# Kernel optimization log

Measured on AMD Instinct MI355X. Metric: run time of the kernel, lower is better.

## Reference

```python
import jax, jax.numpy as jnp
import numpy as np

N_ENT = 100000
N_REL = 500
IN_DIM = 128
OUT_DIM = 128
E = 500000


def setup_inputs() -> dict:
    key = jax.random.key(0)
    ks = jax.random.split(key, 9)
    src = jax.random.randint(ks[0], (E,), 0, N_ENT)
    dst = jax.random.randint(ks[1], (E,), 0, N_ENT)
    rel = jax.random.randint(ks[2], (E,), 0, N_REL)
    ent_embed = jax.random.normal(ks[3], (N_ENT, IN_DIM), dtype=jnp.float32)
    rel_embed = jax.random.normal(ks[4], (N_REL, IN_DIM), dtype=jnp.float32)
    # xavier_normal with gain 1.414 for linear weights
    g = 1.414
    a_w = jax.random.normal(ks[5], (OUT_DIM, 3 * IN_DIM), dtype=jnp.float32) * (g * np.sqrt(2.0 / (3 * IN_DIM + OUT_DIM)))
    a_b = jnp.zeros((OUT_DIM,), dtype=jnp.float32)
    a2_w = jax.random.normal(ks[6], (1, OUT_DIM), dtype=jnp.float32) * (g * np.sqrt(2.0 / (OUT_DIM + 1)))
    a2_b = jnp.zeros((1,), dtype=jnp.float32)
    return {"ent_embed": ent_embed, "rel_embed": rel_embed, "a_w": a_w, "a_b": a_b,
            "a2_w": a2_w, "a2_b": a2_b, "src": src, "dst": dst, "rel": rel}


def reference(ent_embed, rel_embed, a_w, a_b, a2_w, a2_b, src, dst, rel):
    # gather: [E, 3*in_dim]
    h = jnp.concatenate([ent_embed[src], ent_embed[dst], rel_embed[rel]], axis=1)
    c = h @ a_w.T + a_b                      # [E, out_dim]
    b = jax.nn.leaky_relu(c @ a2_w.T + a2_b, negative_slope=0.01)  # [E, 1]
    e_b = jnp.exp(b)                          # [E, 1]
    temp1 = e_b * c                           # [E, out_dim]
    # scatter-sum into source nodes (SpecialSpmmFinal keyed on edges[0] = src)
    e_b_sum = jax.ops.segment_sum(e_b, src, num_segments=N_ENT)   # [N, 1]
    h_sum = jax.ops.segment_sum(temp1, src, num_segments=N_ENT)   # [N, out_dim]
    ebs = jnp.where(e_b_sum == 0, jnp.float32(1e-12), e_b_sum)
    h_ent = h_sum / ebs
    # scatter-mean of temp1 by relation id
    rel_sum = jax.ops.segment_sum(temp1, rel, num_segments=N_REL)          # [R, out_dim]
    rel_cnt = jax.ops.segment_sum(jnp.ones((temp1.shape[0],), jnp.float32), rel, num_segments=N_REL)
    h_rel = rel_sum / jnp.maximum(rel_cnt, 1.0)[:, None]
    return (jax.nn.elu(h_ent), jax.nn.elu(h_rel))
```

## Files before the change

kernel.cpp:

```cpp
#include <hip/hip_runtime.h>
#include <hip/hip_bf16.h>

#define N_ENT_C 100000
#define N_REL_C 500
#define NEDGE_C 500000
#define SCAN_BLOCKS 391
#define EPB 1024
#define NB_EDGE 489
#define CHUNK_B 62
#define MT_TOTAL 6250
#define MT_PER_BLOCK 8
#define MFMA_GRID 782
#define CVT_GRID 1563

#define OFF_WTHI  0
#define OFF_WTLO  16384
#define OFF_WTR   32768
#define OFF_PR    49152
#define OFF_PRH   113152
#define OFF_QR    145920
#define OFF_QS    146432
#define OFF_QD    246432
#define OFF_OSRC  346432
#define OFF_DSTS  446432
#define OFF_RELS  946432
#define OFF_PSH   1446432
#define OFF_PDH   7846432

#define DO_HSRC     0
#define DO_BSUM     100000
#define DO_RELSTART 100512
#define DO_PART8    101024
#define DO_CHUNKOFF 105120
#define DO_BLKHIST  109216
#define DO_BLKOFFS  359584
#define DO_SRCR     609952
#define DO_DSTR     1109952
#define DO_RELP     1609952

typedef short bf16x8 __attribute__((ext_vector_type(8)));
typedef float f32x4  __attribute__((ext_vector_type(4)));
typedef unsigned short u16x8 __attribute__((ext_vector_type(8)));

__device__ inline unsigned short bf_rne(float x) {
    unsigned int u = __float_as_uint(x);
    u += 0x7FFF + ((u >> 16) & 1);
    return (unsigned short)(u >> 16);
}
__device__ inline float bf2f(unsigned short h) {
    return __uint_as_float(((unsigned int)h) << 16);
}

__global__ void prep_w(const float* __restrict__ aw, unsigned short* __restrict__ Wthi,
                       unsigned short* __restrict__ Wtlo, float* __restrict__ Wtr) {
    int idx = blockIdx.x * 256 + threadIdx.x;
    if (idx < 32768) {
        int n = idx >> 7, k = idx & 127;
        float v = (n < 128) ? aw[n * 384 + k] : aw[(n - 128) * 384 + 128 + k];
        unsigned short h = bf_rne(v);
        Wthi[idx] = h;
        Wtlo[idx] = bf_rne(v - bf2f(h));
    } else if (idx < 49152) {
        int t = idx - 32768;
        int k = t >> 7, o = t & 127;
        Wtr[t] = aw[o * 384 + 256 + k];
    }
}

__global__ void rel_proj(const float* __restrict__ rele, const float* __restrict__ Wtr,
                         const float* __restrict__ ab, const float* __restrict__ a2w,
                         float* __restrict__ Pr, unsigned short* __restrict__ PrH,
                         float* __restrict__ qr) {
    int r = blockIdx.x;
    int o = threadIdx.x;
    float acc = ab[o];
    for (int k = 0; k < 128; ++k)
        acc = fmaf(rele[r * 128 + k], Wtr[k * 128 + o], acc);
    Pr[r * 128 + o] = acc;
    PrH[r * 128 + o] = bf_rne(acc);
    __shared__ float red[128];
    red[o] = acc * a2w[o];
    __syncthreads();
    for (int off = 64; off > 0; off >>= 1) {
        if (o < off) red[o] += red[o + off];
        __syncthreads();
    }
    if (o == 0) qr[r] = red[0];
}

__global__ __launch_bounds__(256) void ent_cvt(const float* __restrict__ ent,
                                               uint4* __restrict__ EntF) {
    int gw = blockIdx.x * 256 + threadIdx.x;
    int mt = gw >> 6;
    if (mt >= MT_TOTAL) return;
    int lane = gw & 63;
    int row = mt * 16 + (lane & 15);
    int kb0 = (lane >> 4) * 8;
    const float* rp = ent + (size_t)row * 128;
    size_t mb = (size_t)mt * 8;
#pragma unroll
    for (int ks = 0; ks < 4; ++ks) {
        float4 a = *(const float4*)(rp + ks * 32 + kb0);
        float4 b = *(const float4*)(rp + ks * 32 + kb0 + 4);
        float f[8] = {a.x, a.y, a.z, a.w, b.x, b.y, b.z, b.w};
        union { unsigned short u[8]; uint4 v; } H, L;
#pragma unroll
        for (int j = 0; j < 8; ++j) {
            unsigned short h = bf_rne(f[j]);
            H.u[j] = h;
            L.u[j] = bf_rne(f[j] - bf2f(h));
        }
        EntF[(mb + ks) * 64 + lane] = H.v;
        EntF[(mb + 4 + ks) * 64 + lane] = L.v;
    }
}

__global__ __launch_bounds__(512, 4) void ent_mfma3(const uint4* __restrict__ EntF,
                                                    const unsigned short* __restrict__ Wthi,
                                                    const unsigned short* __restrict__ Wtlo,
                                                    const float* __restrict__ a2w,
                                                    unsigned short* __restrict__ PsH,
                                                    unsigned short* __restrict__ PdH,
                                                    float* __restrict__ qs,
                                                    float* __restrict__ qd) {
    const int tid = threadIdx.x;
    const int w = tid >> 6, lane = tid & 63;
    const int l15 = lane & 15, lh = lane >> 4;
    const int n0 = w * 32;

    bf16x8 wh[2][4], wl[2][4];
#pragma unroll
    for (int nf = 0; nf < 2; ++nf) {
        int n = n0 + nf * 16 + l15;
#pragma unroll
        for (int ks = 0; ks < 4; ++ks) {
            int kb = ks * 32 + lh * 8;
            wh[nf][ks] = *(const bf16x8*)(Wthi + n * 128 + kb);
            wl[nf][ks] = *(const bf16x8*)(Wtlo + n * 128 + kb);
        }
    }
#pragma unroll
    for (int nf = 0; nf < 2; ++nf)
#pragma unroll
        for (int ks = 0; ks < 4; ++ks) {
            asm volatile("" : "+v"(wh[nf][ks]));
            asm volatile("" : "+v"(wl[nf][ks]));
        }

    float a2v[2][4];
#pragma unroll
    for (int nf = 0; nf < 2; ++nf)
#pragma unroll
        for (int v = 0; v < 4; ++v)
            a2v[nf][v] = a2w[(n0 + nf * 16 + lh * 4 + v) & 127];

    const bool isPs = (w < 4);
    unsigned short* PH = isPs ? PsH : PdH;
    float* qout = isPs ? qs : qd;
    const int colbase = (n0 & 127) + lh * 4;

    const bf16x8* EB = (const bf16x8*)EntF;
    f32x4 zz = {0.f, 0.f, 0.f, 0.f};
    const int mt0 = blockIdx.x * MT_PER_BLOCK;

#pragma unroll
    for (int i = 0; i < MT_PER_BLOCK; ++i) {
        int mt = mt0 + i;
        if (mt >= MT_TOTAL) break;
        size_t mb = (size_t)mt * 512;
        bf16x8 eh[4], el[4];
#pragma unroll
        for (int ks = 0; ks < 4; ++ks) {
            eh[ks] = EB[mb + (size_t)ks * 64 + lane];
            el[ks] = EB[mb + 256 + (size_t)ks * 64 + lane];
        }
        f32x4 acc[2];
        acc[0] = zz; acc[1] = zz;
#pragma unroll
        for (int ks = 0; ks < 4; ++ks)
#pragma unroll
            for (int nf = 0; nf < 2; ++nf) {
                acc[nf] = __builtin_amdgcn_mfma_f32_16x16x32_bf16(wh[nf][ks], eh[ks], acc[nf], 0, 0, 0);
                acc[nf] = __builtin_amdgcn_mfma_f32_16x16x32_bf16(wh[nf][ks], el[ks], acc[nf], 0, 0, 0);
                acc[nf] = __builtin_amdgcn_mfma_f32_16x16x32_bf16(wl[nf][ks], eh[ks], acc[nf], 0, 0, 0);
            }

        int m = mt * 16 + l15;
        float qp = 0.f;
#pragma unroll
        for (int nf = 0; nf < 2; ++nf) {
            ushort4 st;
            st.x = bf_rne(acc[nf][0]);
            st.y = bf_rne(acc[nf][1]);
            st.z = bf_rne(acc[nf][2]);
            st.w = bf_rne(acc[nf][3]);
#pragma unroll
            for (int v = 0; v < 4; ++v) qp = fmaf(acc[nf][v], a2v[nf][v], qp);
            *(ushort4*)&PH[(size_t)m * 128 + colbase + nf * 16] = st;
        }
        qp += __shfl_xor(qp, 16);
        qp += __shfl_xor(qp, 32);
        if (lane < 16) unsafeAtomicAdd(&qout[m], qp);
    }
}

__global__ __launch_bounds__(256) void edge_hist(const int* __restrict__ src,
                                                 const int* __restrict__ rel,
                                                 int* __restrict__ histSrc,
                                                 int* __restrict__ blkHist) {
    __shared__ int lh[512];
    int tid = threadIdx.x;
    lh[tid] = 0; lh[tid + 256] = 0;
    __syncthreads();
    int base = blockIdx.x * EPB;
#pragma unroll
    for (int j = 0; j < 4; ++j) {
        int e = base + j * 256 + tid;
        if (e < NEDGE_C) {
            atomicAdd(&histSrc[src[e]], 1);
            atomicAdd(&lh[rel[e]], 1);
        }
    }
    __syncthreads();
    blkHist[blockIdx.x * 512 + tid] = lh[tid];
    blkHist[blockIdx.x * 512 + 256 + tid] = lh[tid + 256];
}

__global__ void colsum(const int* __restrict__ blkHist, int* __restrict__ partial) {
    int r = threadIdx.x;
    int k = blockIdx.x;
    int b0 = k * CHUNK_B;
    int b1 = min(b0 + CHUNK_B, NB_EDGE);
    int t = 0;
    for (int b = b0; b < b1; ++b) t += blkHist[b * 512 + r];
    partial[k * 512 + r] = t;
}

__global__ void scan512(const int* __restrict__ partial, int* __restrict__ relStart,
                        int* __restrict__ chunkOff) {
    __shared__ int a[512], b2[512];
    int tid = threadIdx.x;
    int p8[8];
    int t = 0;
#pragma unroll
    for (int k = 0; k < 8; ++k) { p8[k] = partial[k * 512 + tid]; t += p8[k]; }
    a[tid] = t;
    __syncthreads();
    int v = t;
    int* cur = a; int* nxt = b2;
    for (int off = 1; off < 512; off <<= 1) {
        int x = cur[tid] + ((tid >= off) ? cur[tid - off] : 0);
        nxt[tid] = x;
        __syncthreads();
        int* tmp = cur; cur = nxt; nxt = tmp;
    }
    int excl = cur[tid] - v;
    relStart[tid] = excl;
    int run = excl;
#pragma unroll
    for (int k = 0; k < 8; ++k) { chunkOff[k * 512 + tid] = run; run += p8[k]; }
}

__global__ void colscan(const int* __restrict__ blkHist, const int* __restrict__ chunkOff,
                        int* __restrict__ blockOffs) {
    int r = threadIdx.x;
    int k = blockIdx.x;
    int b0 = k * CHUNK_B;
    int b1 = min(b0 + CHUNK_B, NB_EDGE);
    int off = chunkOff[k * 512 + r];
    for (int b = b0; b < b1; ++b) {
        blockOffs[b * 512 + r] = off;
        off += blkHist[b * 512 + r];
    }
}

__global__ void scan_blockred(const int* __restrict__ hist, int* __restrict__ blockSums, int n) {
    __shared__ int s[256];
    int tid = threadIdx.x;
    int i = blockIdx.x * 256 + tid;
    s[tid] = (i < n) ? hist[i] : 0;
    __syncthreads();
    for (int off = 128; off > 0; off >>= 1) {
        if (tid < off) s[tid] += s[tid + off];
        __syncthreads();
    }
    if (tid == 0) blockSums[blockIdx.x] = s[0];
}

__global__ void scan_single(int* __restrict__ data, int n) {
    __shared__ int a[1024], b2[1024];
    int tid = threadIdx.x;
    int v = (tid < n) ? data[tid] : 0;
    a[tid] = v;
    __syncthreads();
    int* cur = a; int* nxt = b2;
    for (int off = 1; off < 1024; off <<= 1) {
        int x = cur[tid] + ((tid >= off) ? cur[tid - off] : 0);
        nxt[tid] = x;
        __syncthreads();
        int* t = cur; cur = nxt; nxt = t;
    }
    if (tid < n) data[tid] = cur[tid] - v;
}

__global__ void scan_final(const int* __restrict__ hist, const int* __restrict__ blockOffs,
                           int* __restrict__ offs, int n) {
    __shared__ int a[256], b2[256];
    int tid = threadIdx.x;
    int i = blockIdx.x * 256 + tid;
    int v = (i < n) ? hist[i] : 0;
    a[tid] = v;
    __syncthreads();
    int* cur = a; int* nxt = b2;
    for (int off = 1; off < 256; off <<= 1) {
        int x = cur[tid] + ((tid >= off) ? cur[tid - off] : 0);
        nxt[tid] = x;
        __syncthreads();
        int* t = cur; cur = nxt; nxt = t;
    }
    if (i < n) offs[i] = cur[tid] - v + blockOffs[blockIdx.x];
}

__global__ __launch_bounds__(256) void scatter_both(const int* __restrict__ src,
                                                    const int* __restrict__ dst,
                                                    const int* __restrict__ rel,
                                                    int* __restrict__ offsSrc,
                                                    const int* __restrict__ blockOffs,
                                                    int* __restrict__ dstS, int* __restrict__ relS,
                                                    int* __restrict__ srcR, int* __restrict__ dstR) {
    __shared__ int lh[512];
    int tid = threadIdx.x;
    lh[tid] = 0; lh[tid + 256] = 0;
    __syncthreads();
    int base = blockIdx.x * EPB;
    const int* bo = &blockOffs[blockIdx.x * 512];
#pragma unroll
    for (int j = 0; j < 4; ++j) {
        int e = base + j * 256 + tid;
        if (e < NEDGE_C) {
            int s = src[e], d = dst[e], r = rel[e];
            int p = atomicAdd(&offsSrc[s], 1);
            dstS[p] = d; relS[p] = r;
            int lr = atomicAdd(&lh[r], 1);
            int q = bo[r] + lr;
            srcR[q] = s; dstR[q] = d;
        }
    }
}

__global__ __launch_bounds__(256) void rel_phase(const unsigned short* __restrict__ PsH,
                                                 const unsigned short* __restrict__ PdH,
                                                 const float* __restrict__ qs,
                                                 const float* __restrict__ qd,
                                                 const float* __restrict__ qr,
                                                 const int* __restrict__ relStart,
                                                 const int* __restrict__ srcR,
                                                 const int* __restrict__ dstR,
                                                 const float* __restrict__ a2b,
                                                 float* __restrict__ relpart) {
    int r = blockIdx.x >> 3;
    int p = blockIdx.x & 7;
    int start = relStart[r];
    int end = relStart[r + 1];
    int tid = threadIdx.x;
    int w = tid >> 6;
    int h = (tid >> 5) & 1;
    int l = tid & 31;
    int slot = p * 8 + w * 2 + h;
    float bb = a2b[0];
    float qrr = qr[r];
    float4 acc = make_float4(0.f, 0.f, 0.f, 0.f);
    float ebs = 0.f;
    for (int i = start + slot; i < end; i += 64) {
        int s = srcR[i], d = dstR[i];
        float b = qs[s] + qd[d] + qrr + bb;
        b = (b > 0.f) ? b : 0.01f * b;
        float eb = expf(b);
        ushort4 pv = *(const ushort4*)&PsH[(size_t)s * 128 + l * 4];
        ushort4 dv = *(const ushort4*)&PdH[(size_t)d * 128 + l * 4];
        acc.x = fmaf(eb, bf2f(pv.x) + bf2f(dv.x), acc.x);
        acc.y = fmaf(eb, bf2f(pv.y) + bf2f(dv.y), acc.y);
        acc.z = fmaf(eb, bf2f(pv.z) + bf2f(dv.z), acc.z);
        acc.w = fmaf(eb, bf2f(pv.w) + bf2f(dv.w), acc.w);
        ebs += eb;
    }
    __shared__ float vred[8][128];
    __shared__ float sred[8];
    int sub = w * 2 + h;
    *(float4*)&vred[sub][l * 4] = acc;
    if (l == 0) sred[sub] = ebs;
    __syncthreads();
    if (tid < 128) {
        float v = 0.f;
#pragma unroll
        for (int k2 = 0; k2 < 8; ++k2) v += vred[k2][tid];
        float e = 0.f;
#pragma unroll
        for (int k2 = 0; k2 < 8; ++k2) e += sred[k2];
        int pi = r * 8 + p;
        relpart[pi * 132 + tid] = v;
        if (tid == 0) relpart[pi * 132 + 128] = e;
    }
}

__global__ void rel_fin(const float* __restrict__ relpart, const float* __restrict__ Pr,
                        const int* __restrict__ relStart, float* __restrict__ outRel) {
    int r = blockIdx.x;
    int o = threadIdx.x;
    float v = 0.f, e = 0.f;
#pragma unroll
    for (int p = 0; p < 8; ++p) {
        v += relpart[(r * 8 + p) * 132 + o];
        e += relpart[(r * 8 + p) * 132 + 128];
    }
    float cnt = (float)(relStart[r + 1] - relStart[r]);
    float h = (v + e * Pr[r * 128 + o]) / fmaxf(cnt, 1.f);
    outRel[r * 128 + o] = (h > 0.f) ? h : (expf(h) - 1.f);
}

__global__ __launch_bounds__(256) void src_phase(const unsigned short* __restrict__ PsH,
                                                 const unsigned short* __restrict__ PdH,
                                                 const unsigned short* __restrict__ PrH,
                                                 const float* __restrict__ qs,
                                                 const float* __restrict__ qd,
                                                 const float* __restrict__ qr,
                                                 const int* __restrict__ offsSrc,
                                                 const int* __restrict__ dstS,
                                                 const int* __restrict__ relS,
                                                 const float* __restrict__ a2b,
                                                 float* __restrict__ out) {
    int wid = (blockIdx.x * 256 + threadIdx.x) >> 6;
    if (wid >= N_ENT_C) return;
    int lane = threadIdx.x & 63;
    int g = lane >> 4, l = lane & 15;
    int s = wid;
    int start = (s == 0) ? 0 : offsSrc[s - 1];
    int end = offsSrc[s];
    float* dstp = &out[(size_t)s * 128];
    if (end == start) {
        if (g == 0) {
            *(float4*)&dstp[l * 8] = make_float4(0.f, 0.f, 0.f, 0.f);
            *(float4*)&dstp[l * 8 + 4] = make_float4(0.f, 0.f, 0.f, 0.f);
        }
        return;
    }
    float bb = a2b[0];
    float qss = qs[s];
    float acc[8];
#pragma unroll
    for (int j = 0; j < 8; ++j) acc[j] = 0.f;
    float ebs = 0.f;
    for (int i = start + g; i < end; i += 4) {
        int d = dstS[i], r = relS[i];
        float b = qss + qd[d] + qr[r] + bb;
        b = (b > 0.f) ? b : 0.01f * b;
        float eb = expf(b);
        u16x8 dv = *(const u16x8*)&PdH[(size_t)d * 128 + l * 8];
        u16x8 rv = *(const u16x8*)&PrH[(size_t)r * 128 + l * 8];
#pragma unroll
        for (int j = 0; j < 8; ++j)
            acc[j] = fmaf(eb, bf2f(dv[j]) + bf2f(rv[j]), acc[j]);
        ebs += eb;
    }
#pragma unroll
    for (int j = 0; j < 8; ++j) {
        acc[j] += __shfl_xor(acc[j], 16);
        acc[j] += __shfl_xor(acc[j], 32);
    }
    ebs += __shfl_xor(ebs, 16);
    ebs += __shfl_xor(ebs, 32);
    if (g == 0) {
        float inv = 1.f / ebs;
        u16x8 ps = *(const u16x8*)&PsH[(size_t)s * 128 + l * 8];
        float h[8];
#pragma unroll
        for (int j = 0; j < 8; ++j) {
            float x = bf2f(ps[j]) + acc[j] * inv;
            h[j] = (x > 0.f) ? x : (expf(x) - 1.f);
        }
        *(float4*)&dstp[l * 8]     = make_float4(h[0], h[1], h[2], h[3]);
        *(float4*)&dstp[l * 8 + 4] = make_float4(h[4], h[5], h[6], h[7]);
    }
}

extern "C" void kernel_launch(void* const* d_in, const int* in_sizes, int n_in,
                              void* d_out, int out_size, void* d_ws, size_t ws_size,
                              hipStream_t stream) {
    const float* ent  = (const float*)d_in[0];
    const float* rele = (const float*)d_in[1];
    const float* aw   = (const float*)d_in[2];
    const float* ab   = (const float*)d_in[3];
    const float* a2w  = (const float*)d_in[4];
    const float* a2b  = (const float*)d_in[5];
    const int* src    = (const int*)d_in[6];
    const int* dst    = (const int*)d_in[7];
    const int* rel    = (const int*)d_in[8];
    float* out = (float*)d_out;

    float* ws = (float*)d_ws;
    unsigned short* Wthi = (unsigned short*)(ws + OFF_WTHI);
    unsigned short* Wtlo = (unsigned short*)(ws + OFF_WTLO);
    float* Wtr = ws + OFF_WTR;
    float* Pr  = ws + OFF_PR;
    unsigned short* PrH = (unsigned short*)(ws + OFF_PRH);
    float* qr  = ws + OFF_QR;
    float* qs  = ws + OFF_QS;
    float* qd  = ws + OFF_QD;
    int* offsSrc = (int*)(ws + OFF_OSRC);
    int* dstS    = (int*)(ws + OFF_DSTS);
    int* relS    = (int*)(ws + OFF_RELS);
    unsigned short* PsH = (unsigned short*)(ws + OFF_PSH);
    unsigned short* PdH = (unsigned short*)(ws + OFF_PDH);

    int* dI = (int*)d_out;
    uint4* EntF   = (uint4*)d_out;
    int* histSrc  = dI + DO_HSRC;
    int* bsum     = dI + DO_BSUM;
    int* relStart = dI + DO_RELSTART;
    int* part8    = dI + DO_PART8;
    int* chunkOff = dI + DO_CHUNKOFF;
    int* blkHist  = dI + DO_BLKHIST;
    int* blockOffs= dI + DO_BLKOFFS;
    int* srcR     = dI + DO_SRCR;
    int* dstR     = dI + DO_DSTR;
    float* relpart = (float*)dI + DO_RELP;

    hipMemsetAsync(ws + OFF_QR, 0, (size_t)(OFF_OSRC - OFF_QR) * sizeof(float), stream);

    prep_w<<<192, 256, 0, stream>>>(aw, Wthi, Wtlo, Wtr);
    rel_proj<<<N_REL_C, 128, 0, stream>>>(rele, Wtr, ab, a2w, Pr, PrH, qr);
    ent_cvt<<<CVT_GRID, 256, 0, stream>>>(ent, EntF);
    ent_mfma3<<<MFMA_GRID, 512, 0, stream>>>(EntF, Wthi, Wtlo, a2w, PsH, PdH, qs, qd);

    hipMemsetAsync(histSrc, 0, (size_t)N_ENT_C * sizeof(int), stream);
    edge_hist<<<NB_EDGE, 256, 0, stream>>>(src, rel, histSrc, blkHist);
    colsum<<<8, 512, 0, stream>>>(blkHist, part8);
    scan512<<<1, 512, 0, stream>>>(part8, relStart, chunkOff);
    colscan<<<8, 512, 0, stream>>>(blkHist, chunkOff, blockOffs);
    scan_blockred<<<SCAN_BLOCKS, 256, 0, stream>>>(histSrc, bsum, N_ENT_C);
    scan_single<<<1, 1024, 0, stream>>>(bsum, SCAN_BLOCKS);
    scan_final<<<SCAN_BLOCKS, 256, 0, stream>>>(histSrc, bsum, offsSrc, N_ENT_C);
    scatter_both<<<NB_EDGE, 256, 0, stream>>>(src, dst, rel, offsSrc, blockOffs,
                                              dstS, relS, srcR, dstR);

    rel_phase<<<N_REL_C * 8, 256, 0, stream>>>(PsH, PdH, qs, qd, qr, relStart, srcR, dstR,
                                               a2b, relpart);
    rel_fin<<<N_REL_C, 128, 0, stream>>>(relpart, Pr, relStart, out + (size_t)N_ENT_C * 128);

    src_phase<<<(N_ENT_C + 3) / 4, 256, 0, stream>>>(PsH, PdH, PrH, qs, qd, qr,
                                                     offsSrc, dstS, relS, a2b, out);
}
```

Measured before the change: 273.5 us.

## Pack edge index pairs as int2 and widen src_phase to eight edge groups

The separate dst/rel and src/dst index arrays become interleaved int2 arrays, so scatter writes and phase reads touch one 8-byte slot per edge instead of two separate arrays. src_phase now has each wave process 8 edges in parallel with 8 lanes covering 16 features each, instead of 4 edges with 16 lanes of 8 features. The aim is more independent gathers in flight per wave, since nodes average about 5 edges. The cost is twice the accumulator registers, an extra shuffle stage, and idle lane groups for low-degree nodes. The PsH load is also hoisted ahead of the loop.

```diff
diff --git a/kernel.cpp b/kernel.cpp
--- a/kernel.cpp
+++ b/kernel.cpp
@@ -22,8 +22,7 @@
 #define OFF_QS    146432
 #define OFF_QD    246432
 #define OFF_OSRC  346432
-#define OFF_DSTS  446432
-#define OFF_RELS  946432
+#define OFF_DRS   446432
 #define OFF_PSH   1446432
 #define OFF_PDH   7846432
 
@@ -34,8 +33,7 @@
 #define DO_CHUNKOFF 105120
 #define DO_BLKHIST  109216
 #define DO_BLKOFFS  359584
-#define DO_SRCR     609952
-#define DO_DSTR     1109952
+#define DO_SDR      609952
 #define DO_RELP     1609952
 
 typedef short bf16x8 __attribute__((ext_vector_type(8)));
@@ -326,8 +324,8 @@
                                                     const int* __restrict__ rel,
                                                     int* __restrict__ offsSrc,
                                                     const int* __restrict__ blockOffs,
-                                                    int* __restrict__ dstS, int* __restrict__ relS,
-                                                    int* __restrict__ srcR, int* __restrict__ dstR) {
+                                                    int2* __restrict__ drS,
+                                                    int2* __restrict__ sdR) {
     __shared__ int lh[512];
     int tid = threadIdx.x;
     lh[tid] = 0; lh[tid + 256] = 0;
@@ -340,10 +338,9 @@
         if (e < NEDGE_C) {
             int s = src[e], d = dst[e], r = rel[e];
             int p = atomicAdd(&offsSrc[s], 1);
-            dstS[p] = d; relS[p] = r;
+            drS[p] = make_int2(d, r);
             int lr = atomicAdd(&lh[r], 1);
-            int q = bo[r] + lr;
-            srcR[q] = s; dstR[q] = d;
+            sdR[bo[r] + lr] = make_int2(s, d);
         }
     }
 }
@@ -354,8 +351,7 @@
                                                  const float* __restrict__ qd,
                                                  const float* __restrict__ qr,
                                                  const int* __restrict__ relStart,
-                                                 const int* __restrict__ srcR,
-                                                 const int* __restrict__ dstR,
+                                                 const int2* __restrict__ sdR,
                                                  const float* __restrict__ a2b,
                                                  float* __restrict__ relpart) {
     int r = blockIdx.x >> 3;
@@ -372,7 +368,8 @@
     float4 acc = make_float4(0.f, 0.f, 0.f, 0.f);
     float ebs = 0.f;
     for (int i = start + slot; i < end; i += 64) {
-        int s = srcR[i], d = dstR[i];
+        int2 sd = sdR[i];
+        int s = sd.x, d = sd.y;
         float b = qs[s] + qd[d] + qrr + bb;
         b = (b > 0.f) ? b : 0.01f * b;
         float eb = expf(b);
@@ -425,61 +422,76 @@
                                                  const float* __restrict__ qd,
                                                  const float* __restrict__ qr,
                                                  const int* __restrict__ offsSrc,
-                                                 const int* __restrict__ dstS,
-                                                 const int* __restrict__ relS,
+                                                 const int2* __restrict__ drS,
                                                  const float* __restrict__ a2b,
                                                  float* __restrict__ out) {
     int wid = (blockIdx.x * 256 + threadIdx.x) >> 6;
     if (wid >= N_ENT_C) return;
     int lane = threadIdx.x & 63;
-    int g = lane >> 4, l = lane & 15;
+    int g = lane >> 3, l = lane & 7;
     int s = wid;
     int start = (s == 0) ? 0 : offsSrc[s - 1];
     int end = offsSrc[s];
     float* dstp = &out[(size_t)s * 128];
     if (end == start) {
         if (g == 0) {
-            *(float4*)&dstp[l * 8] = make_float4(0.f, 0.f, 0.f, 0.f);
-            *(float4*)&dstp[l * 8 + 4] = make_float4(0.f, 0.f, 0.f, 0.f);
+#pragma unroll
+            for (int q = 0; q < 4; ++q)
+                *(float4*)&dstp[l * 16 + q * 4] = make_float4(0.f, 0.f, 0.f, 0.f);
         }
         return;
     }
     float bb = a2b[0];
     float qss = qs[s];
-    float acc[8];
-#pragma unroll
-    for (int j = 0; j < 8; ++j) acc[j] = 0.f;
+    u16x8 ps0, ps1;
+    if (g == 0) {
+        ps0 = *(const u16x8*)&PsH[(size_t)s * 128 + l * 16];
+        ps1 = *(const u16x8*)&PsH[(size_t)s * 128 + l * 16 + 8];
+    }
+    float acc[16];
+#pragma unroll
+    for (int j = 0; j < 16; ++j) acc[j] = 0.f;
     float ebs = 0.f;
-    for (int i = start + g; i < end; i += 4) {
-        int d = dstS[i], r = relS[i];
+    for (int i = start + g; i < end; i += 8) {
+        int2 dr = drS[i];
+        int d = dr.x, r = dr.y;
         float b = qss + qd[d] + qr[r] + bb;
         b = (b > 0.f) ? b : 0.01f * b;
         float eb = expf(b);
-        u16x8 dv = *(const u16x8*)&PdH[(size_t)d * 128 + l * 8];
-        u16x8 rv = *(const u16x8*)&PrH[(size_t)r * 128 + l * 8];
-#pragma unroll
-        for (int j = 0; j < 8; ++j)
-            acc[j] = fmaf(eb, bf2f(dv[j]) + bf2f(rv[j]), acc[j]);
+        u16x8 dv0 = *(const u16x8*)&PdH[(size_t)d * 128 + l * 16];
+        u16x8 dv1 = *(const u16x8*)&PdH[(size_t)d * 128 + l * 16 + 8];
+        u16x8 rv0 = *(const u16x8*)&PrH[(size_t)r * 128 + l * 16];
+        u16x8 rv1 = *(const u16x8*)&PrH[(size_t)r * 128 + l * 16 + 8];
+#pragma unroll
+        for (int j = 0; j < 8; ++j) {
+            acc[j]     = fmaf(eb, bf2f(dv0[j]) + bf2f(rv0[j]), acc[j]);
+            acc[8 + j] = fmaf(eb, bf2f(dv1[j]) + bf2f(rv1[j]), acc[8 + j]);
+        }
         ebs += eb;
     }
 #pragma unroll
-    for (int j = 0; j < 8; ++j) {
+    for (int j = 0; j < 16; ++j) {
+        acc[j] += __shfl_xor(acc[j], 8);
         acc[j] += __shfl_xor(acc[j], 16);
         acc[j] += __shfl_xor(acc[j], 32);
     }
+    ebs += __shfl_xor(ebs, 8);
     ebs += __shfl_xor(ebs, 16);
     ebs += __shfl_xor(ebs, 32);
     if (g == 0) {
         float inv = 1.f / ebs;
-        u16x8 ps = *(const u16x8*)&PsH[(size_t)s * 128 + l * 8];
-        float h[8];
+        float h[16];
 #pragma unroll
         for (int j = 0; j < 8; ++j) {
-            float x = bf2f(ps[j]) + acc[j] * inv;
-            h[j] = (x > 0.f) ? x : (expf(x) - 1.f);
-        }
-        *(float4*)&dstp[l * 8]     = make_float4(h[0], h[1], h[2], h[3]);
-        *(float4*)&dstp[l * 8 + 4] = make_float4(h[4], h[5], h[6], h[7]);
+            float x0 = bf2f(ps0[j]) + acc[j] * inv;
+            float x1 = bf2f(ps1[j]) + acc[8 + j] * inv;
+            h[j]     = (x0 > 0.f) ? x0 : (expf(x0) - 1.f);
+            h[8 + j] = (x1 > 0.f) ? x1 : (expf(x1) - 1.f);
+        }
+        *(float4*)&dstp[l * 16]      = make_float4(h[0], h[1], h[2], h[3]);
+        *(float4*)&dstp[l * 16 + 4]  = make_float4(h[4], h[5], h[6], h[7]);
+        *(float4*)&dstp[l * 16 + 8]  = make_float4(h[8], h[9], h[10], h[11]);
+        *(float4*)&dstp[l * 16 + 12] = make_float4(h[12], h[13], h[14], h[15]);
     }
 }
 
@@ -507,8 +519,7 @@
     float* qs  = ws + OFF_QS;
     float* qd  = ws + OFF_QD;
     int* offsSrc = (int*)(ws + OFF_OSRC);
-    int* dstS    = (int*)(ws + OFF_DSTS);
-    int* relS    = (int*)(ws + OFF_RELS);
+    int2* drS    = (int2*)(ws + OFF_DRS);
     unsigned short* PsH = (unsigned short*)(ws + OFF_PSH);
     unsigned short* PdH = (unsigned short*)(ws + OFF_PDH);
 
@@ -521,8 +532,7 @@
     int* chunkOff = dI + DO_CHUNKOFF;
     int* blkHist  = dI + DO_BLKHIST;
     int* blockOffs= dI + DO_BLKOFFS;
-    int* srcR     = dI + DO_SRCR;
-    int* dstR     = dI + DO_DSTR;
+    int2* sdR     = (int2*)(dI + DO_SDR);
     float* relpart = (float*)dI + DO_RELP;
 
     hipMemsetAsync(ws + OFF_QR, 0, (size_t)(OFF_OSRC - OFF_QR) * sizeof(float), stream);
@@ -540,13 +550,12 @@
     scan_blockred<<<SCAN_BLOCKS, 256, 0, stream>>>(histSrc, bsum, N_ENT_C);
     scan_single<<<1, 1024, 0, stream>>>(bsum, SCAN_BLOCKS);
     scan_final<<<SCAN_BLOCKS, 256, 0, stream>>>(histSrc, bsum, offsSrc, N_ENT_C);
-    scatter_both<<<NB_EDGE, 256, 0, stream>>>(src, dst, rel, offsSrc, blockOffs,
-                                              dstS, relS, srcR, dstR);
-
-    rel_phase<<<N_REL_C * 8, 256, 0, stream>>>(PsH, PdH, qs, qd, qr, relStart, srcR, dstR,
+    scatter_both<<<NB_EDGE, 256, 0, stream>>>(src, dst, rel, offsSrc, blockOffs, drS, sdR);
+
+    rel_phase<<<N_REL_C * 8, 256, 0, stream>>>(PsH, PdH, qs, qd, qr, relStart, sdR,
                                                a2b, relpart);
     rel_fin<<<N_REL_C, 128, 0, stream>>>(relpart, Pr, relStart, out + (size_t)N_ENT_C * 128);
 
     src_phase<<<(N_ENT_C + 3) / 4, 256, 0, stream>>>(PsH, PdH, PrH, qs, qd, qr,
-                                                     offsSrc, dstS, relS, a2b, out);
-}
+                                                     offsSrc, drS, a2b, out);
+}
```

After: 295.6 us. +8.0%, slower.
